# Kernel optimization log

Hardware: AMD Instinct MI355X
Metric: run time of the kernel (lower is better)

Reference implementation:

```python
import jax, jax.numpy as jnp
import numpy as np

DIM = 512
WS = 8
NH = 16
HD = DIM // NH
N = WS * WS
B = 2048
SCALE = HD ** -0.5


def _rel_pos_index(ws):
    # Swin relative position index for a ws x ws window -> [N*N] int indices
    coords = np.stack(np.meshgrid(np.arange(ws), np.arange(ws), indexing='ij')).reshape(2, -1)
    rel = coords[:, :, None] - coords[:, None, :]          # [2, N, N]
    rel = rel.transpose(1, 2, 0).copy()                    # [N, N, 2]
    rel[..., 0] += ws - 1
    rel[..., 1] += ws - 1
    rel[..., 0] *= 2 * ws - 1
    return rel.sum(-1).reshape(-1)                         # [N*N]

REL_IDX = jnp.asarray(_rel_pos_index(WS))


def setup_inputs() -> dict:
    key = jax.random.key(0)
    ks = jax.random.split(key, 6)
    x = jax.random.normal(ks[0], (B, N, DIM), dtype=jnp.float32)
    W_qkv = jax.random.normal(ks[1], (3 * DIM, DIM), dtype=jnp.float32) * 0.02
    b_qkv = jnp.zeros((3 * DIM,), dtype=jnp.float32)
    W_proj = jax.random.normal(ks[2], (DIM, DIM), dtype=jnp.float32) * 0.02
    b_proj = jnp.zeros((DIM,), dtype=jnp.float32)
    bias_table = jax.random.normal(ks[3], ((2 * WS - 1) * (2 * WS - 1), NH), dtype=jnp.float32) * 0.02
    return {"x": x, "W_qkv": W_qkv, "b_qkv": b_qkv, "W_proj": W_proj, "b_proj": b_proj, "bias_table": bias_table}


def reference(x, W_qkv, b_qkv, W_proj, b_proj, bias_table):
    B_, n, c = x.shape
    qkv = x @ W_qkv.T + b_qkv                              # [B, N, 3C]
    qkv = qkv.reshape(B_, n, 3, NH, HD)
    q = qkv[:, :, 0].transpose(0, 2, 1, 3)                 # [B, H, N, hd]
    k = qkv[:, :, 1].transpose(0, 2, 1, 3)
    v = qkv[:, :, 2].transpose(0, 2, 1, 3)
    attn = jnp.einsum('bhnd,bhmd->bhnm', q, k) * SCALE     # [B, H, N, N]
    bias = bias_table[REL_IDX].reshape(n, n, NH).transpose(2, 0, 1)  # [H, N, N]
    attn = jax.nn.softmax(attn + bias[None], axis=-1)
    out = jnp.einsum('bhnm,bhmd->bhnd', attn, v)           # [B, H, N, hd]
    out = out.transpose(0, 2, 1, 3).reshape(B_, n, c)      # [B, N, C]
    return out @ W_proj.T + b_proj
```

## Files before the change

kernel.cpp:

```cpp
#include <hip/hip_runtime.h>
#include <stdint.h>

#define NHEADS 16
#define HDIM 32
#define NTOK 64
#define NWIN_B 2048
#define MROWS (NWIN_B * NTOK)
#define CDIM 512
#define QKVDIM 1536
#define ATT_SCALE 0.17677669529663687f

typedef __attribute__((ext_vector_type(8))) short short8;
typedef __attribute__((ext_vector_type(4))) float f32x4;

__device__ __forceinline__ unsigned short f2bf(float f) {
  unsigned int u = __float_as_uint(f);
  u += 0x7FFFu + ((u >> 16) & 1u);
  return (unsigned short)(u >> 16);
}

__device__ __forceinline__ void gload_lds16(const unsigned short* g, unsigned short* l) {
  __builtin_amdgcn_global_load_lds(
      (const __attribute__((address_space(1))) unsigned int*)g,
      (__attribute__((address_space(3))) unsigned int*)l, 16, 0, 0);
}

__global__ void cvt_bf16_kernel(const float* __restrict__ src,
                                unsigned short* __restrict__ dst, int n4) {
  int i = blockIdx.x * blockDim.x + threadIdx.x;
  if (i >= n4) return;
  const float4 v = ((const float4*)src)[i];
  ushort4 o;
  o.x = f2bf(v.x); o.y = f2bf(v.y); o.z = f2bf(v.z); o.w = f2bf(v.w);
  ((ushort4*)dst)[i] = o;
}

__global__ void expand_bias_kernel(const float* __restrict__ table,
                                   float* __restrict__ biasx) {
  const int t = blockIdx.x * blockDim.x + threadIdx.x;
  const int col = t & 63, row = (t >> 6) & 63, h = t >> 12;
  const int idx = ((row >> 3) - (col >> 3) + 7) * 15 + ((row & 7) - (col & 7) + 7);
  biasx[t] = table[idx * NHEADS + h];
}

template <typename OutT>
__global__ __launch_bounds__(256) void gemm_bt_kernel(
    const unsigned short* __restrict__ A,
    const unsigned short* __restrict__ Bt,
    const float* __restrict__ bias,
    OutT* __restrict__ C, int M, int N, int K) {
  constexpr int BM = 128, BN = 128, BK = 64;
  __shared__ __align__(16) unsigned short As[BM * BK];
  __shared__ __align__(16) unsigned short Bs[BN * BK];

  const int tid = threadIdx.x;
  const int w = tid >> 6, lane = tid & 63;
  const int quad = lane >> 4, l16 = lane & 15;
  const int wr = w >> 1, wc = w & 1;
  const long rowBase = (long)blockIdx.y * BM;
  const long colBase = (long)blockIdx.x * BN;

  const int srow = w * 32 + (lane >> 3);
  const int scol = (lane & 7) * 8;

  f32x4 acc[4][4] = {};

  for (int k0 = 0; k0 < K; k0 += BK) {
#pragma unroll
    for (int i = 0; i < 4; ++i) {
      const int r = srow + i * 8;
      gload_lds16(A  + (rowBase + r) * K + k0 + scol, &As[(w * 32 + i * 8) * BK]);
      gload_lds16(Bt + (colBase + r) * K + k0 + scol, &Bs[(w * 32 + i * 8) * BK]);
    }
    __syncthreads();
#pragma unroll
    for (int kk = 0; kk < BK; kk += 32) {
      short8 aF[4], bF[4];
#pragma unroll
      for (int t = 0; t < 4; ++t)
        aF[t] = *(const short8*)&As[(wr * 64 + t * 16 + l16) * BK + kk + quad * 8];
#pragma unroll
      for (int t = 0; t < 4; ++t)
        bF[t] = *(const short8*)&Bs[(wc * 64 + t * 16 + l16) * BK + kk + quad * 8];
#pragma unroll
      for (int mt = 0; mt < 4; ++mt)
#pragma unroll
        for (int nt = 0; nt < 4; ++nt)
          acc[mt][nt] = __builtin_amdgcn_mfma_f32_16x16x32_bf16(
              aF[mt], bF[nt], acc[mt][nt], 0, 0, 0);
    }
    __syncthreads();
  }

#pragma unroll
  for (int nt = 0; nt < 4; ++nt) {
    const long col = colBase + wc * 64 + nt * 16 + l16;
    const float bv = bias[col];
#pragma unroll
    for (int mt = 0; mt < 4; ++mt) {
      const long row0 = rowBase + wr * 64 + mt * 16 + quad * 4;
#pragma unroll
      for (int r = 0; r < 4; ++r) {
        const float v = acc[mt][nt][r] + bv;
        if constexpr (sizeof(OutT) == 2)
          C[(row0 + r) * N + col] = (OutT)f2bf(v);
        else
          C[(row0 + r) * N + col] = (OutT)v;
      }
    }
  }
}

__global__ __launch_bounds__(256) void attn_kernel(
    const unsigned short* __restrict__ qkv,
    const float* __restrict__ biasx,
    unsigned short* __restrict__ aout) {
  __shared__ __align__(16) unsigned short P[4][NTOK * 72];

  const int tid = threadIdx.x;
  const int w = tid >> 6, lane = tid & 63;
  const int quad = lane >> 4, l16 = lane & 15;
  const int b = blockIdx.x >> 2;
  const int h = (blockIdx.x & 3) * 4 + w;

  const unsigned short* base = qkv + (long)b * NTOK * QKVDIM;
  const int hoff = h * HDIM;

  short8 qF[4], kF[4];
#pragma unroll
  for (int t = 0; t < 4; ++t) {
    const long roff = (long)(t * 16 + l16) * QKVDIM;
    qF[t] = *(const short8*)(base + roff + hoff + quad * 8);
    kF[t] = *(const short8*)(base + roff + 512 + hoff + quad * 8);
  }

  f32x4 S[4][4];
#pragma unroll
  for (int mi = 0; mi < 4; ++mi)
#pragma unroll
    for (int ni = 0; ni < 4; ++ni) {
      f32x4 z = {0.f, 0.f, 0.f, 0.f};
      S[mi][ni] = __builtin_amdgcn_mfma_f32_16x16x32_bf16(qF[mi], kF[ni], z, 0, 0, 0);
    }

  const float* bh = biasx + h * (NTOK * NTOK);
#pragma unroll
  for (int mi = 0; mi < 4; ++mi) {
#pragma unroll
    for (int r = 0; r < 4; ++r) {
      const int row = mi * 16 + quad * 4 + r;
      float vals[4], mx = -3.4e38f;
#pragma unroll
      for (int ni = 0; ni < 4; ++ni) {
        const float s = S[mi][ni][r] * ATT_SCALE + bh[row * 64 + ni * 16 + l16];
        vals[ni] = s;
        mx = fmaxf(mx, s);
      }
#pragma unroll
      for (int d = 1; d < 16; d <<= 1) mx = fmaxf(mx, __shfl_xor(mx, d));
      float sum = 0.f;
#pragma unroll
      for (int ni = 0; ni < 4; ++ni) { vals[ni] = __expf(vals[ni] - mx); sum += vals[ni]; }
#pragma unroll
      for (int d = 1; d < 16; d <<= 1) sum += __shfl_xor(sum, d);
      const float inv = 1.0f / sum;
#pragma unroll
      for (int ni = 0; ni < 4; ++ni)
        P[w][row * 72 + ni * 16 + l16] = f2bf(vals[ni] * inv);
    }
  }

  short8 vF[2][2];
#pragma unroll
  for (int kt = 0; kt < 2; ++kt)
#pragma unroll
    for (int dt = 0; dt < 2; ++dt) {
      short8 f;
#pragma unroll
      for (int j = 0; j < 8; ++j) {
        const int n = kt * 32 + quad * 8 + j;
        f[j] = (short)base[(long)n * QKVDIM + 1024 + hoff + dt * 16 + l16];
      }
      vF[kt][dt] = f;
    }

  __syncthreads();

  f32x4 O[4][2] = {};
#pragma unroll
  for (int mi = 0; mi < 4; ++mi)
#pragma unroll
    for (int kt = 0; kt < 2; ++kt) {
      const short8 pF = *(const short8*)&P[w][(mi * 16 + l16) * 72 + kt * 32 + quad * 8];
#pragma unroll
      for (int dt = 0; dt < 2; ++dt)
        O[mi][dt] = __builtin_amdgcn_mfma_f32_16x16x32_bf16(pF, vF[kt][dt], O[mi][dt], 0, 0, 0);
    }

#pragma unroll
  for (int mi = 0; mi < 4; ++mi)
#pragma unroll
    for (int dt = 0; dt < 2; ++dt)
#pragma unroll
      for (int r = 0; r < 4; ++r) {
        const int row = mi * 16 + quad * 4 + r;
        aout[((long)b * NTOK + row) * CDIM + hoff + dt * 16 + l16] = f2bf(O[mi][dt][r]);
      }
}

extern "C" void kernel_launch(void* const* d_in, const int* in_sizes, int n_in,
                              void* d_out, int out_size, void* d_ws, size_t ws_size,
                              hipStream_t stream) {
  const float* x      = (const float*)d_in[0];
  const float* W_qkv  = (const float*)d_in[1];
  const float* b_qkv  = (const float*)d_in[2];
  const float* W_proj = (const float*)d_in[3];
  const float* b_proj = (const float*)d_in[4];
  const float* btab   = (const float*)d_in[5];

  char* ws = (char*)d_ws;
  unsigned short* qkv   = (unsigned short*)ws;
  unsigned short* xb    = (unsigned short*)(ws + 402653184L);
  unsigned short* aout  = xb;
  unsigned short* wqkvb = (unsigned short*)(ws + 402653184L + 134217728L);
  unsigned short* wprjb = (unsigned short*)(ws + 402653184L + 134217728L + 1572864L);
  float*          biasx = (float*)(ws + 402653184L + 134217728L + 1572864L + 524288L);

  cvt_bf16_kernel<<<(MROWS * CDIM) / 1024, 256, 0, stream>>>(x, xb, (MROWS * CDIM) / 4);
  cvt_bf16_kernel<<<(QKVDIM * CDIM) / 1024, 256, 0, stream>>>(W_qkv, wqkvb, (QKVDIM * CDIM) / 4);
  cvt_bf16_kernel<<<(CDIM * CDIM) / 1024, 256, 0, stream>>>(W_proj, wprjb, (CDIM * CDIM) / 4);
  expand_bias_kernel<<<(NHEADS * NTOK * NTOK) / 256, 256, 0, stream>>>(btab, biasx);

  gemm_bt_kernel<unsigned short><<<dim3(QKVDIM / 128, MROWS / 128), 256, 0, stream>>>(
      xb, wqkvb, b_qkv, qkv, MROWS, QKVDIM, CDIM);

  attn_kernel<<<NWIN_B * 4, 256, 0, stream>>>(qkv, biasx, aout);

  gemm_bt_kernel<float><<<dim3(CDIM / 128, MROWS / 128), 256, 0, stream>>>(
      aout, wprjb, b_proj, (float*)d_out, MROWS, CDIM, CDIM);
}
```

Baseline: 1.165 ms.

## Swizzle LDS tiles, remap GEMM blocks per XCD, stage attention QKV through LDS

The GEMM now XOR-swizzles the LDS layout of its A/B tiles to avoid bank conflicts. It remaps a flat 1D grid so each XCD gets a contiguous band of row blocks, which improves L2 reuse. For bf16 output it stages the tile in LDS and writes it back with coalesced 16-byte stores. The attention kernel loads its 128-column Q/K/V slices into a swizzled LDS buffer with async global-to-LDS loads instead of strided per-lane global reads, at the cost of more shared memory per block and lower occupancy.

```diff
diff --git a/kernel.cpp b/kernel.cpp
--- a/kernel.cpp
+++ b/kernel.cpp
@@ -48,40 +48,48 @@
     const unsigned short* __restrict__ A,
     const unsigned short* __restrict__ Bt,
     const float* __restrict__ bias,
-    OutT* __restrict__ C, int M, int N, int K) {
+    OutT* __restrict__ C, int M, int N, int K, int nxb) {
   constexpr int BM = 128, BN = 128, BK = 64;
-  __shared__ __align__(16) unsigned short As[BM * BK];
-  __shared__ __align__(16) unsigned short Bs[BN * BK];
+  __shared__ __align__(16) unsigned short smem[BM * BK + BN * BK];
+  unsigned short* As = smem;
+  unsigned short* Bs = smem + BM * BK;
 
   const int tid = threadIdx.x;
   const int w = tid >> 6, lane = tid & 63;
   const int quad = lane >> 4, l16 = lane & 15;
   const int wr = w >> 1, wc = w & 1;
-  const long rowBase = (long)blockIdx.y * BM;
-  const long colBase = (long)blockIdx.x * BN;
-
-  const int srow = w * 32 + (lane >> 3);
-  const int scol = (lane & 7) * 8;
+
+  const int nyb_per_xcd = (gridDim.x / nxb) >> 3;
+  const int xcd = blockIdx.x & 7;
+  const int idx = blockIdx.x >> 3;
+  const long rowBase = (long)(xcd * nyb_per_xcd + idx / nxb) * BM;
+  const long colBase = (long)(idx % nxb) * BN;
+
+  const int srow8 = lane >> 3;
+  const int gchunk = (lane & 7) ^ srow8;
+
+  const long aBase0 = (rowBase + w * 32 + srow8) * (long)K + gchunk * 8;
+  const long bBase0 = (colBase + w * 32 + srow8) * (long)K + gchunk * 8;
 
   f32x4 acc[4][4] = {};
 
   for (int k0 = 0; k0 < K; k0 += BK) {
 #pragma unroll
     for (int i = 0; i < 4; ++i) {
-      const int r = srow + i * 8;
-      gload_lds16(A  + (rowBase + r) * K + k0 + scol, &As[(w * 32 + i * 8) * BK]);
-      gload_lds16(Bt + (colBase + r) * K + k0 + scol, &Bs[(w * 32 + i * 8) * BK]);
+      gload_lds16(A  + aBase0 + (long)(i * 8) * K + k0, &As[(w * 32 + i * 8) * BK]);
+      gload_lds16(Bt + bBase0 + (long)(i * 8) * K + k0, &Bs[(w * 32 + i * 8) * BK]);
     }
     __syncthreads();
 #pragma unroll
-    for (int kk = 0; kk < BK; kk += 32) {
+    for (int kkc = 0; kkc < 2; ++kkc) {
+      const int p = ((quad + kkc * 4) ^ (l16 & 7)) * 8;
       short8 aF[4], bF[4];
 #pragma unroll
       for (int t = 0; t < 4; ++t)
-        aF[t] = *(const short8*)&As[(wr * 64 + t * 16 + l16) * BK + kk + quad * 8];
+        aF[t] = *(const short8*)&As[(wr * 64 + t * 16 + l16) * BK + p];
 #pragma unroll
       for (int t = 0; t < 4; ++t)
-        bF[t] = *(const short8*)&Bs[(wc * 64 + t * 16 + l16) * BK + kk + quad * 8];
+        bF[t] = *(const short8*)&Bs[(wc * 64 + t * 16 + l16) * BK + p];
 #pragma unroll
       for (int mt = 0; mt < 4; ++mt)
 #pragma unroll
@@ -92,20 +100,39 @@
     __syncthreads();
   }
 
-#pragma unroll
-  for (int nt = 0; nt < 4; ++nt) {
-    const long col = colBase + wc * 64 + nt * 16 + l16;
-    const float bv = bias[col];
-#pragma unroll
-    for (int mt = 0; mt < 4; ++mt) {
-      const long row0 = rowBase + wr * 64 + mt * 16 + quad * 4;
-#pragma unroll
-      for (int r = 0; r < 4; ++r) {
-        const float v = acc[mt][nt][r] + bv;
-        if constexpr (sizeof(OutT) == 2)
-          C[(row0 + r) * N + col] = (OutT)f2bf(v);
-        else
-          C[(row0 + r) * N + col] = (OutT)v;
+  if constexpr (sizeof(OutT) == 2) {
+    unsigned short* Cs = smem;
+#pragma unroll
+    for (int nt = 0; nt < 4; ++nt) {
+      const int col = wc * 64 + nt * 16 + l16;
+      const float bv = bias[colBase + col];
+#pragma unroll
+      for (int mt = 0; mt < 4; ++mt) {
+        const int row0 = wr * 64 + mt * 16 + quad * 4;
+#pragma unroll
+        for (int r = 0; r < 4; ++r)
+          Cs[(row0 + r) * 128 + col] = f2bf(acc[mt][nt][r] + bv);
+      }
+    }
+    __syncthreads();
+#pragma unroll
+    for (int t = 0; t < 8; ++t) {
+      const int ci = t * 256 + tid;
+      const int row = ci >> 4, ch = ci & 15;
+      *(short8*)((unsigned short*)C + (rowBase + row) * N + colBase + ch * 8) =
+          *(const short8*)&Cs[ci * 8];
+    }
+  } else {
+#pragma unroll
+    for (int nt = 0; nt < 4; ++nt) {
+      const long col = colBase + wc * 64 + nt * 16 + l16;
+      const float bv = bias[col];
+#pragma unroll
+      for (int mt = 0; mt < 4; ++mt) {
+        const long row0 = rowBase + wr * 64 + mt * 16 + quad * 4;
+#pragma unroll
+        for (int r = 0; r < 4; ++r)
+          C[(row0 + r) * N + col] = acc[mt][nt][r] + bv;
       }
     }
   }
@@ -115,23 +142,38 @@
     const unsigned short* __restrict__ qkv,
     const float* __restrict__ biasx,
     unsigned short* __restrict__ aout) {
-  __shared__ __align__(16) unsigned short P[4][NTOK * 72];
+  __shared__ __align__(16) unsigned short sT[3 * 64 * 128];
+  unsigned short* P = sT;
 
   const int tid = threadIdx.x;
   const int w = tid >> 6, lane = tid & 63;
   const int quad = lane >> 4, l16 = lane & 15;
   const int b = blockIdx.x >> 2;
-  const int h = (blockIdx.x & 3) * 4 + w;
-
-  const unsigned short* base = qkv + (long)b * NTOK * QKVDIM;
-  const int hoff = h * HDIM;
+  const int q = blockIdx.x & 3;
+  const int h = q * 4 + w;
+
+  const unsigned short* base = qkv + (long)b * NTOK * QKVDIM + q * 128;
+
+  const int rloc = lane >> 4;
+  const int ch = lane & 15;
+#pragma unroll
+  for (int t = 0; t < 3; ++t) {
+#pragma unroll
+    for (int i = 0; i < 4; ++i) {
+      const int r = w * 16 + i * 4 + rloc;
+      const int gc = ch ^ (r & 15);
+      gload_lds16(base + (long)r * QKVDIM + t * 512 + gc * 8,
+                  &sT[t * 8192 + (w * 16 + i * 4) * 128]);
+    }
+  }
+  __syncthreads();
 
   short8 qF[4], kF[4];
+  const int pQ = ((w * 4 + quad) ^ l16) * 8;
 #pragma unroll
   for (int t = 0; t < 4; ++t) {
-    const long roff = (long)(t * 16 + l16) * QKVDIM;
-    qF[t] = *(const short8*)(base + roff + hoff + quad * 8);
-    kF[t] = *(const short8*)(base + roff + 512 + hoff + quad * 8);
+    qF[t] = *(const short8*)&sT[0 * 8192 + (t * 16 + l16) * 128 + pQ];
+    kF[t] = *(const short8*)&sT[1 * 8192 + (t * 16 + l16) * 128 + pQ];
   }
 
   f32x4 S[4][4];
@@ -142,6 +184,23 @@
       f32x4 z = {0.f, 0.f, 0.f, 0.f};
       S[mi][ni] = __builtin_amdgcn_mfma_f32_16x16x32_bf16(qF[mi], kF[ni], z, 0, 0, 0);
     }
+
+  short8 vF[2][2];
+#pragma unroll
+  for (int kt = 0; kt < 2; ++kt)
+#pragma unroll
+    for (int dt = 0; dt < 2; ++dt) {
+      short8 f;
+#pragma unroll
+      for (int j = 0; j < 8; ++j) {
+        const int n = kt * 32 + quad * 8 + j;
+        const int c = w * 4 + dt * 2 + (l16 >> 3);
+        f[j] = (short)sT[2 * 8192 + n * 128 + (c ^ (n & 15)) * 8 + (l16 & 7)];
+      }
+      vF[kt][dt] = f;
+    }
+
+  __syncthreads();
 
   const float* bh = biasx + h * (NTOK * NTOK);
 #pragma unroll
@@ -166,32 +225,16 @@
       const float inv = 1.0f / sum;
 #pragma unroll
       for (int ni = 0; ni < 4; ++ni)
-        P[w][row * 72 + ni * 16 + l16] = f2bf(vals[ni] * inv);
-    }
-  }
-
-  short8 vF[2][2];
-#pragma unroll
-  for (int kt = 0; kt < 2; ++kt)
-#pragma unroll
-    for (int dt = 0; dt < 2; ++dt) {
-      short8 f;
-#pragma unroll
-      for (int j = 0; j < 8; ++j) {
-        const int n = kt * 32 + quad * 8 + j;
-        f[j] = (short)base[(long)n * QKVDIM + 1024 + hoff + dt * 16 + l16];
-      }
-      vF[kt][dt] = f;
-    }
-
-  __syncthreads();
+        P[w * 4608 + row * 72 + ni * 16 + l16] = f2bf(vals[ni] * inv);
+    }
+  }
 
   f32x4 O[4][2] = {};
 #pragma unroll
   for (int mi = 0; mi < 4; ++mi)
 #pragma unroll
     for (int kt = 0; kt < 2; ++kt) {
-      const short8 pF = *(const short8*)&P[w][(mi * 16 + l16) * 72 + kt * 32 + quad * 8];
+      const short8 pF = *(const short8*)&P[w * 4608 + (mi * 16 + l16) * 72 + kt * 32 + quad * 8];
 #pragma unroll
       for (int dt = 0; dt < 2; ++dt)
         O[mi][dt] = __builtin_amdgcn_mfma_f32_16x16x32_bf16(pF, vF[kt][dt], O[mi][dt], 0, 0, 0);
@@ -204,7 +247,7 @@
 #pragma unroll
       for (int r = 0; r < 4; ++r) {
         const int row = mi * 16 + quad * 4 + r;
-        aout[((long)b * NTOK + row) * CDIM + hoff + dt * 16 + l16] = f2bf(O[mi][dt][r]);
+        aout[((long)b * NTOK + row) * CDIM + h * HDIM + dt * 16 + l16] = f2bf(O[mi][dt][r]);
       }
 }
 
@@ -231,11 +274,11 @@
   cvt_bf16_kernel<<<(CDIM * CDIM) / 1024, 256, 0, stream>>>(W_proj, wprjb, (CDIM * CDIM) / 4);
   expand_bias_kernel<<<(NHEADS * NTOK * NTOK) / 256, 256, 0, stream>>>(btab, biasx);
 
-  gemm_bt_kernel<unsigned short><<<dim3(QKVDIM / 128, MROWS / 128), 256, 0, stream>>>(
-      xb, wqkvb, b_qkv, qkv, MROWS, QKVDIM, CDIM);
+  gemm_bt_kernel<unsigned short><<<(MROWS / 128) * (QKVDIM / 128), 256, 0, stream>>>(
+      xb, wqkvb, b_qkv, qkv, MROWS, QKVDIM, CDIM, QKVDIM / 128);
 
   attn_kernel<<<NWIN_B * 4, 256, 0, stream>>>(qkv, biasx, aout);
 
-  gemm_bt_kernel<float><<<dim3(CDIM / 128, MROWS / 128), 256, 0, stream>>>(
-      aout, wprjb, b_proj, (float*)d_out, MROWS, CDIM, CDIM);
-}
+  gemm_bt_kernel<float><<<(MROWS / 128) * (CDIM / 128), 256, 0, stream>>>(
+      aout, wprjb, b_proj, (float*)d_out, MROWS, CDIM, CDIM, CDIM / 128);
+}
```

Result: faster. 1.011 ms (-13.2%).
